# Optimization experiments

Hardware: AMD Instinct MI355X
Metric: run time of the kernel (lower is better)

## Reference

```python
import jax, jax.numpy as jnp
import numpy as np

N, E = 50000, 500000
G_DIM, H1, H2 = 256, 128, 128
N_REL, N_BASES = 8, 30  # 2 * n_speakers**2 with n_speakers=2


def setup_inputs() -> dict:
    key = jax.random.key(0)
    ks = jax.random.split(key, 12)
    inp = {
        "node_features": jax.random.normal(ks[0], (N, G_DIM), jnp.float32),
        "edge_index": jax.random.randint(ks[1], (2, E), 0, N, jnp.int64),
        "edge_norm": jax.random.uniform(ks[2], (E,), jnp.float32),
        "edge_type": jax.random.randint(ks[3], (E,), 0, N_REL, jnp.int64),
        # RGCNConv (basis decomposition) params
        "basis": jax.random.normal(ks[4], (N_BASES, G_DIM, H1), jnp.float32) / np.sqrt(G_DIM),
        "comp": jax.random.normal(ks[5], (N_REL, N_BASES), jnp.float32) / np.sqrt(N_BASES),
        "root": jax.random.normal(ks[6], (G_DIM, H1), jnp.float32) / np.sqrt(G_DIM),
        "bias1": jnp.zeros((H1,), jnp.float32),
        # GATv2Conv params (heads=1)
        "w_l": jax.random.normal(ks[7], (H1, H2), jnp.float32) / np.sqrt(H1),
        "w_r": jax.random.normal(ks[8], (H1, H2), jnp.float32) / np.sqrt(H1),
        "att": jax.random.normal(ks[9], (H2,), jnp.float32) / np.sqrt(H2),
        "bias2": jnp.zeros((H2,), jnp.float32),
    }
    return inp


def reference(node_features, edge_index, edge_norm, edge_type,
              basis, comp, root, bias1, w_l, w_r, att, bias2):
    # NOTE: edge_norm is accepted but unused, matching the original forward.
    src, dst = edge_index[0], edge_index[1]
    n = node_features.shape[0]
    R = comp.shape[0]

    # ---- RGCNConv with basis decomposition, per-relation mean aggregation ----
    Wr = jnp.einsum('rb,bio->rio', comp, basis)            # [R, g_dim, h1]
    xr = jnp.einsum('ni,rio->nro', node_features, Wr)      # [N, R, h1]
    msg = xr[src, edge_type]                               # [E, h1] gather per edge
    seg = dst * R + edge_type                              # segment = (node, relation)
    sums = jax.ops.segment_sum(msg, seg, num_segments=n * R)
    cnts = jax.ops.segment_sum(jnp.ones((msg.shape[0],), msg.dtype), seg, num_segments=n * R)
    mean = sums / jnp.maximum(cnts, 1.0)[:, None]          # per-(node,relation) mean
    agg = mean.reshape(n, R, -1).sum(axis=1)               # sum over relations
    x1 = agg + node_features @ root + bias1                # [N, h1]

    # ---- GATv2Conv (heads=1, add_self_loops=True) ----
    loop = jnp.arange(n, dtype=src.dtype)
    s2 = jnp.concatenate([src, loop])
    d2 = jnp.concatenate([dst, loop])
    xl = x1 @ w_l                                          # source transform [N, h2]
    xrt = x1 @ w_r                                         # target transform [N, h2]
    e = jax.nn.leaky_relu(xl[s2] + xrt[d2], 0.2) @ att     # [E+N] edge scores
    emax = jax.ops.segment_max(e, d2, num_segments=n)      # self-loops => every seg nonempty
    ex = jnp.exp(e - emax[d2])
    denom = jax.ops.segment_sum(ex, d2, num_segments=n)
    alpha = ex / denom[d2]                                 # segment softmax over incoming edges
    out = jax.ops.segment_sum(alpha[:, None] * xl[s2], d2, num_segments=n) + bias2
    return out
```

## Files before the change

### kernel.cpp

```cpp
#include <hip/hip_runtime.h>
#include <hip/hip_bf16.h>
#include <cstdint>
#include <cstddef>

#define NN 50000
#define NE 500000
#define GD 256
#define H1 128
#define H2 128
#define NREL 8
#define NBASES 30
#define XRLD (NREL * H1)
#define NCHUNKS ((NN + 1023) / 1024)

typedef __attribute__((ext_vector_type(8))) short bf16x8;
typedef __attribute__((ext_vector_type(4))) float f32x4;
typedef __attribute__((ext_vector_type(8))) unsigned short u16x8;

__device__ __forceinline__ float lrelu(float x) { return x > 0.f ? x : 0.2f * x; }

__device__ __forceinline__ unsigned short f2bf(float x) {
  union { float f; uint32_t u; } v; v.f = x;
  uint32_t r = v.u + 0x7FFF + ((v.u >> 16) & 1);
  return (unsigned short)(r >> 16);
}
__device__ __forceinline__ float bf2f(unsigned short u) {
  union { uint32_t u; float f; } v; v.u = ((uint32_t)u) << 16;
  return v.f;
}

template <int N>
__device__ __forceinline__ void wait_vmcnt() {
  asm volatile("s_waitcnt vmcnt(%0)" :: "n"(N) : "memory");
}

__device__ __forceinline__ void gload_lds(const unsigned short* gp, unsigned short* lp) {
  __builtin_amdgcn_global_load_lds(
      (const __attribute__((address_space(1))) void*)gp,
      (__attribute__((address_space(3))) void*)lp, 16, 0, 0);
}

__global__ void k_cast(const float* __restrict__ in, unsigned short* __restrict__ out) {
  int i = blockIdx.x * 256 + threadIdx.x;
  const float4* p = (const float4*)(in + (size_t)i * 8);
  float4 a = p[0], b = p[1];
  u16x8 r;
  r[0] = f2bf(a.x); r[1] = f2bf(a.y); r[2] = f2bf(a.z); r[3] = f2bf(a.w);
  r[4] = f2bf(b.x); r[5] = f2bf(b.y); r[6] = f2bf(b.z); r[7] = f2bf(b.w);
  *(u16x8*)(out + (size_t)i * 8) = r;
}

__global__ void k_wr(const float* __restrict__ basis, const float* __restrict__ comp,
                     unsigned short* __restrict__ wrb_t) {
  int idx = blockIdx.x * 256 + threadIdx.x;
  int n = idx >> 8;
  int k = idx & 255;
  int r = n >> 7, o = n & 127;
  float acc = 0.f;
  #pragma unroll
  for (int b = 0; b < NBASES; b++)
    acc += comp[r * NBASES + b] * basis[((size_t)b * GD + k) * H1 + o];
  wrb_t[idx] = f2bf(acc);
}

__global__ void k_prep(const float* __restrict__ root, const float* __restrict__ w_l,
                       const float* __restrict__ w_r, const float* __restrict__ bias1,
                       unsigned short* __restrict__ btf, float* __restrict__ biasv) {
  int idx = blockIdx.x * 256 + threadIdx.x;
  if (idx < 32768) {
    int c = idx >> 7, k = idx & 127;
    float v = (c < H2) ? w_l[k * H2 + c] : w_r[k * H2 + (c - H2)];
    btf[c * 384 + k] = f2bf(v);
  } else if (idx < 98304) {
    int j2 = idx - 32768;
    int c = j2 >> 8, g = j2 & 255;
    float acc = 0.f;
    for (int j = 0; j < H1; j++) {
      float w = (c < H2) ? w_l[j * H2 + c] : w_r[j * H2 + (c - H2)];
      acc += root[g * H1 + j] * w;
    }
    btf[c * 384 + 128 + g] = f2bf(acc);
  } else if (idx < 98560) {
    int c = idx - 98304;
    float acc = 0.f;
    for (int j = 0; j < H1; j++) {
      float w = (c < H2) ? w_l[j * H2 + c] : w_r[j * H2 + (c - H2)];
      acc += bias1[j] * w;
    }
    biasv[c] = acc;
  }
}

template <int K, int WM>
__global__ __launch_bounds__(256, 3)
void k_mgemm(const unsigned short* __restrict__ A, const unsigned short* __restrict__ Bt,
             unsigned short* __restrict__ C, int M, int N, int gx) {
  constexpr int BM = WM * 32;
  constexpr int ACH = BM * 4;
  constexpr int TCH = ACH + 512;
  constexpr int LPT = TCH / 256;
  constexpr int NS = K / 32;
  constexpr int ABUF = BM * 32;
  constexpr int BBUF = 128 * 32;
  extern __shared__ unsigned short lds[];
  const int tid = threadIdx.x;
  const int lane = tid & 63;
  const int wave = tid >> 6;

  const int nwg = gridDim.x;
  const int q = nwg >> 3, r = nwg & 7;
  const int xcd = blockIdx.x & 7, bi = blockIdx.x >> 3;
  const int wg = (xcd < r ? xcd * (q + 1) : r * (q + 1) + (xcd - r) * q) + bi;
  const int bx = wg % gx;
  const int by = wg / gx;
  const int row0 = by * BM;
  const int colb = bx * 128;
  const int wcol = (wave & 1) * 64;
  const int wrow = (wave >> 1) * (WM * 16);
  const int lr = lane & 15;
  const int lko = lane >> 4;

  f32x4 acc[WM][4];
  #pragma unroll
  for (int i = 0; i < WM; i++)
    #pragma unroll
    for (int j = 0; j < 4; j++) acc[i][j] = (f32x4){0.f, 0.f, 0.f, 0.f};

  auto stage = [&](int k0, int b) {
    unsigned short* as = lds + b * ABUF;
    unsigned short* bs = lds + 3 * ABUF + b * BBUF;
    #pragma unroll
    for (int it = 0; it < LPT; it++) {
      int ci = it * 256 + tid;
      if (ci < ACH) {
        int row = ci >> 2, cs = ci & 3;
        int s = (row & 3) ^ ((row >> 2) & 3);
        int gm = row0 + row; if (gm >= M) gm = M - 1;
        gload_lds(A + (size_t)gm * K + k0 + ((cs ^ s) << 3), as + (size_t)ci * 8);
      } else {
        int cj = ci - ACH;
        int row = cj >> 2, cs = cj & 3;
        int s = (row & 3) ^ ((row >> 2) & 3);
        gload_lds(Bt + (size_t)(colb + row) * K + k0 + ((cs ^ s) << 3), bs + (size_t)cj * 8);
      }
    }
  };

  auto compute = [&](int b) {
    const unsigned short* as = lds + b * ABUF;
    const unsigned short* bs = lds + 3 * ABUF + b * BBUF;
    bf16x8 af[WM], bfr[4];
    #pragma unroll
    for (int mb = 0; mb < WM; mb++) {
      int rowL = wrow + mb * 16 + lr;
      int s = (rowL & 3) ^ ((rowL >> 2) & 3);
      af[mb] = *(const bf16x8*)&as[rowL * 32 + ((lko ^ s) << 3)];
    }
    #pragma unroll
    for (int nb = 0; nb < 4; nb++) {
      int colL = wcol + nb * 16 + lr;
      int s = (colL & 3) ^ ((colL >> 2) & 3);
      bfr[nb] = *(const bf16x8*)&bs[colL * 32 + ((lko ^ s) << 3)];
    }
    #pragma unroll
    for (int mb = 0; mb < WM; mb++)
      #pragma unroll
      for (int nb = 0; nb < 4; nb++)
        acc[mb][nb] = __builtin_amdgcn_mfma_f32_16x16x32_bf16(af[mb], bfr[nb], acc[mb][nb], 0, 0, 0);
  };

  stage(0, 0);
  stage(32, 1);
  wait_vmcnt<LPT>();
  __builtin_amdgcn_sched_barrier(0);
  __builtin_amdgcn_s_barrier();
  #pragma unroll
  for (int s = 0; s < NS; s++) {
    if (s + 2 < NS) stage((s + 2) * 32, (s + 2) % 3);
    compute(s % 3);
    if (s + 1 < NS) {
      if (s + 2 < NS) wait_vmcnt<LPT>();
      else            wait_vmcnt<0>();
      __builtin_amdgcn_sched_barrier(0);
      __builtin_amdgcn_s_barrier();
    }
  }

  __syncthreads();
  unsigned short* Cs = lds;
  const int orow = lko * 4;
  #pragma unroll
  for (int mb = 0; mb < WM; mb++) {
    #pragma unroll
    for (int i = 0; i < 4; i++) {
      int row = wrow + mb * 16 + orow + i;
      int sw = (row & 7) << 3;
      #pragma unroll
      for (int nb = 0; nb < 4; nb++) {
        int col = wcol + nb * 16 + lr;
        Cs[row * 128 + (col ^ sw)] = f2bf(acc[mb][nb][i]);
      }
    }
  }
  __syncthreads();
  #pragma unroll
  for (int it = 0; it < BM / 16; it++) {
    int off = it * 256 + tid;
    int row = off >> 4, jb = off & 15;
    int grow = row0 + row;
    if (grow < M) {
      int idx = row * 128 + ((jb * 8) ^ ((row & 7) << 3));
      *(u16x8*)&C[(size_t)grow * N + colb + jb * 8] = *(const u16x8*)&Cs[idx];
    }
  }
}

__global__ __launch_bounds__(256, 3)
void k_fused(const unsigned short* __restrict__ A1, const unsigned short* __restrict__ A2,
             const unsigned short* __restrict__ Bt, const float* __restrict__ biasv,
             unsigned short* __restrict__ C, int M) {
  constexpr int K = 384, NS = 12, LPT = 4;
  extern __shared__ unsigned short lds[];
  const int tid = threadIdx.x;
  const int lane = tid & 63;
  const int wave = tid >> 6;

  const int nwg = gridDim.x;
  const int q = nwg >> 3, r = nwg & 7;
  const int xcd = blockIdx.x & 7, bi = blockIdx.x >> 3;
  const int wg = (xcd < r ? xcd * (q + 1) : r * (q + 1) + (xcd - r) * q) + bi;
  const int bx = wg & 1;
  const int by = wg >> 1;
  const int row0 = by * 128;
  const int colb = bx * 128;
  const int wcol = (wave & 1) * 64;
  const int wrow = (wave >> 1) * 64;
  const int lr = lane & 15;
  const int lko = lane >> 4;

  f32x4 acc[4][4];
  #pragma unroll
  for (int i = 0; i < 4; i++)
    #pragma unroll
    for (int j = 0; j < 4; j++) acc[i][j] = (f32x4){0.f, 0.f, 0.f, 0.f};

  auto stage = [&](int k0, int b) {
    unsigned short* as = lds + b * 4096;
    unsigned short* bs = lds + 3 * 4096 + b * 4096;
    #pragma unroll
    for (int it = 0; it < LPT; it++) {
      int ci = it * 256 + tid;
      if (ci < 512) {
        int row = ci >> 2, cs = ci & 3;
        int s = (row & 3) ^ ((row >> 2) & 3);
        int gm = row0 + row; if (gm >= M) gm = M - 1;
        const unsigned short* gp;
        if (k0 < 128) gp = A1 + (size_t)gm * 128 + k0 + ((cs ^ s) << 3);
        else          gp = A2 + (size_t)gm * 256 + (k0 - 128) + ((cs ^ s) << 3);
        gload_lds(gp, as + (size_t)ci * 8);
      } else {
        int cj = ci - 512;
        int row = cj >> 2, cs = cj & 3;
        int s = (row & 3) ^ ((row >> 2) & 3);
        gload_lds(Bt + (size_t)(colb + row) * K + k0 + ((cs ^ s) << 3), bs + (size_t)cj * 8);
      }
    }
  };

  auto compute = [&](int b) {
    const unsigned short* as = lds + b * 4096;
    const unsigned short* bs = lds + 3 * 4096 + b * 4096;
    bf16x8 af[4], bfr[4];
    #pragma unroll
    for (int mb = 0; mb < 4; mb++) {
      int rowL = wrow + mb * 16 + lr;
      int s = (rowL & 3) ^ ((rowL >> 2) & 3);
      af[mb] = *(const bf16x8*)&as[rowL * 32 + ((lko ^ s) << 3)];
    }
    #pragma unroll
    for (int nb = 0; nb < 4; nb++) {
      int colL = wcol + nb * 16 + lr;
      int s = (colL & 3) ^ ((colL >> 2) & 3);
      bfr[nb] = *(const bf16x8*)&bs[colL * 32 + ((lko ^ s) << 3)];
    }
    #pragma unroll
    for (int mb = 0; mb < 4; mb++)
      #pragma unroll
      for (int nb = 0; nb < 4; nb++)
        acc[mb][nb] = __builtin_amdgcn_mfma_f32_16x16x32_bf16(af[mb], bfr[nb], acc[mb][nb], 0, 0, 0);
  };

  stage(0, 0);
  stage(32, 1);
  wait_vmcnt<LPT>();
  __builtin_amdgcn_sched_barrier(0);
  __builtin_amdgcn_s_barrier();
  #pragma unroll
  for (int s = 0; s < NS; s++) {
    if (s + 2 < NS) stage((s + 2) * 32, (s + 2) % 3);
    compute(s % 3);
    if (s + 1 < NS) {
      if (s + 2 < NS) wait_vmcnt<LPT>();
      else            wait_vmcnt<0>();
      __builtin_amdgcn_sched_barrier(0);
      __builtin_amdgcn_s_barrier();
    }
  }

  __syncthreads();
  unsigned short* Cs = lds;
  const int orow = lko * 4;
  #pragma unroll
  for (int mb = 0; mb < 4; mb++) {
    #pragma unroll
    for (int i = 0; i < 4; i++) {
      int row = wrow + mb * 16 + orow + i;
      int sw = (row & 7) << 3;
      #pragma unroll
      for (int nb = 0; nb < 4; nb++) {
        int col = wcol + nb * 16 + lr;
        Cs[row * 128 + (col ^ sw)] = f2bf(acc[mb][nb][i] + biasv[colb + col]);
      }
    }
  }
  __syncthreads();
  #pragma unroll
  for (int it = 0; it < 8; it++) {
    int off = it * 256 + tid;
    int row = off >> 4, jb = off & 15;
    int grow = row0 + row;
    if (grow < M) {
      int idx = row * 128 + ((jb * 8) ^ ((row & 7) << 3));
      *(u16x8*)&C[(size_t)grow * 256 + colb + jb * 8] = *(const u16x8*)&Cs[idx];
    }
  }
}

__global__ void k_deg(const int* __restrict__ ei, const int* __restrict__ et,
                      int* __restrict__ cnt2) {
  int e = blockIdx.x * 256 + threadIdx.x;
  if (e < NE) atomicAdd(&cnt2[ei[NE + e] * NREL + et[e]], 1);
}

__device__ __forceinline__ int node_deg(const int* cnt2, int n) {
  const int4* p = (const int4*)(cnt2 + n * NREL);
  int4 a = p[0], b = p[1];
  return a.x + a.y + a.z + a.w + b.x + b.y + b.z + b.w;
}

__global__ void k_scan_a(const int* __restrict__ cnt2, int* __restrict__ parts) {
  __shared__ int lds[256];
  int t = threadIdx.x;
  int base = blockIdx.x * 1024 + t * 4;
  int s = 0;
  #pragma unroll
  for (int j = 0; j < 4; j++) s += (base + j < NN) ? node_deg(cnt2, base + j) : 0;
  lds[t] = s;
  __syncthreads();
  for (int st = 128; st > 0; st >>= 1) {
    if (t < st) lds[t] += lds[t + st];
    __syncthreads();
  }
  if (t == 0) parts[blockIdx.x] = lds[0];
}

__global__ void k_scan_b(int* __restrict__ parts) {
  int t = threadIdx.x;
  int v = (t < NCHUNKS) ? parts[t] : 0;
  int x = v;
  #pragma unroll
  for (int off = 1; off < 64; off <<= 1) {
    int y = __shfl_up(x, off, 64);
    if (t >= off) x += y;
  }
  if (t < NCHUNKS) parts[t] = x - v;
}

__global__ void k_scan_c(const int* __restrict__ cnt2, const int* __restrict__ parts,
                         int* __restrict__ rowptr) {
  __shared__ int lds[256];
  int t = threadIdx.x;
  int base = blockIdx.x * 1024 + t * 4;
  int v[4];
  int s = 0;
  #pragma unroll
  for (int j = 0; j < 4; j++) { v[j] = (base + j < NN) ? node_deg(cnt2, base + j) : 0; s += v[j]; }
  lds[t] = s;
  __syncthreads();
  for (int st = 1; st < 256; st <<= 1) {
    int add = (t >= st) ? lds[t - st] : 0;
    __syncthreads();
    lds[t] += add;
    __syncthreads();
  }
  int excl = lds[t] - s;
  int off = parts[blockIdx.x];
  int run = 0;
  #pragma unroll
  for (int j = 0; j < 4; j++) {
    run += v[j];
    if (base + j < NN) rowptr[base + j + 1] = off + excl + run;
  }
  if (blockIdx.x == 0 && t == 0) rowptr[0] = 0;
}

__global__ void k_scatter(const int* __restrict__ ei, const int* __restrict__ et,
                          const int* __restrict__ rowptr, const int* __restrict__ cnt2,
                          int* __restrict__ cursor, int* __restrict__ csr,
                          float* __restrict__ wgt) {
  int e = blockIdx.x * 256 + threadIdx.x;
  if (e < NE) {
    int d = ei[NE + e];
    int r = et[e];
    int pos = atomicAdd(&cursor[d], 1);
    int slot = rowptr[d] + pos;
    csr[slot] = ei[e] | (r << 20);
    wgt[slot] = 1.0f / (float)cnt2[d * NREL + r];
  }
}

__global__ __launch_bounds__(256)
void k_rgcn(const unsigned short* __restrict__ xr, const int* __restrict__ csr2,
            const float* __restrict__ wgt, const int* __restrict__ rowptr,
            unsigned short* __restrict__ agg) {
  int wpair = (blockIdx.x * 256 + threadIdx.x) >> 6;
  int lane = threadIdx.x & 63;
  int hb = lane & 32;
  int l = lane & 31;
  int wid = wpair * 2 + (hb >> 5);
  if (wid >= NN) return;
  int c0 = l * 4;
  float a0 = 0.f, a1 = 0.f, a2 = 0.f, a3 = 0.f;
  int beg = rowptr[wid], end = rowptr[wid + 1];
  for (int j0 = beg; j0 < end; j0 += 32) {
    int nv = end - j0; if (nv > 32) nv = 32;
    int pk = (l < nv) ? csr2[j0 + l] : 0;
    float wk = (l < nv) ? wgt[j0 + l] : 0.f;
    int t = 0;
    for (; t + 8 <= nv; t += 8) {
      uint2 wv[8]; float wz[8];
      #pragma unroll
      for (int z = 0; z < 8; z++) {
        int p = __shfl(pk, hb + t + z, 64);
        wz[z] = __shfl(wk, hb + t + z, 64);
        size_t off = (size_t)(p & 0xFFFFF) * XRLD + (p >> 20) * H1 + c0;
        wv[z] = *(const uint2*)(xr + off);
      }
      #pragma unroll
      for (int z = 0; z < 8; z++) {
        a0 += wz[z] * bf2f((unsigned short)(wv[z].x & 0xffff));
        a1 += wz[z] * bf2f((unsigned short)(wv[z].x >> 16));
        a2 += wz[z] * bf2f((unsigned short)(wv[z].y & 0xffff));
        a3 += wz[z] * bf2f((unsigned short)(wv[z].y >> 16));
      }
    }
    for (; t < nv; t++) {
      int p = __shfl(pk, hb + t, 64);
      float w = __shfl(wk, hb + t, 64);
      size_t off = (size_t)(p & 0xFFFFF) * XRLD + (p >> 20) * H1 + c0;
      uint2 wv = *(const uint2*)(xr + off);
      a0 += w * bf2f((unsigned short)(wv.x & 0xffff));
      a1 += w * bf2f((unsigned short)(wv.x >> 16));
      a2 += w * bf2f((unsigned short)(wv.y & 0xffff));
      a3 += w * bf2f((unsigned short)(wv.y >> 16));
    }
  }
  uint2 packed;
  packed.x = (uint32_t)f2bf(a0) | ((uint32_t)f2bf(a1) << 16);
  packed.y = (uint32_t)f2bf(a2) | ((uint32_t)f2bf(a3) << 16);
  *(uint2*)&agg[(size_t)wid * H1 + c0] = packed;
}

__global__ __launch_bounds__(256)
void k_gat(const unsigned short* __restrict__ xlr, const int* __restrict__ csr2,
           const int* __restrict__ rowptr, const float* __restrict__ att,
           const float* __restrict__ bias2, float* __restrict__ out) {
  int wpair = (blockIdx.x * 256 + threadIdx.x) >> 6;
  int lane = threadIdx.x & 63;
  int hb = lane & 32;
  int l = lane & 31;
  int wid = wpair * 2 + (hb >> 5);
  if (wid >= NN) return;
  int c0 = l * 4;
  float4 at = *(const float4*)(att + c0);
  uint2 wr2 = *(const uint2*)(xlr + (size_t)wid * 256 + 128 + c0);
  float xr0 = bf2f((unsigned short)(wr2.x & 0xffff));
  float xr1 = bf2f((unsigned short)(wr2.x >> 16));
  float xr2 = bf2f((unsigned short)(wr2.y & 0xffff));
  float xr3 = bf2f((unsigned short)(wr2.y >> 16));
  uint2 wv0 = *(const uint2*)(xlr + (size_t)wid * 256 + c0);
  float v0 = bf2f((unsigned short)(wv0.x & 0xffff));
  float v1 = bf2f((unsigned short)(wv0.x >> 16));
  float v2 = bf2f((unsigned short)(wv0.y & 0xffff));
  float v3 = bf2f((unsigned short)(wv0.y >> 16));
  float ep = lrelu(v0 + xr0) * at.x + lrelu(v1 + xr1) * at.y +
             lrelu(v2 + xr2) * at.z + lrelu(v3 + xr3) * at.w;
  #pragma unroll
  for (int off = 16; off > 0; off >>= 1) ep += __shfl_xor(ep, off, 64);
  float m = ep, s = 1.f, o0 = v0, o1 = v1, o2 = v2, o3 = v3;
  int beg = rowptr[wid], end = rowptr[wid + 1];
  for (int j0 = beg; j0 < end; j0 += 32) {
    int nv = end - j0; if (nv > 32) nv = 32;
    int pk = (l < nv) ? csr2[j0 + l] : 0;
    int t = 0;
    for (; t + 8 <= nv; t += 8) {
      float u0[8], u1[8], u2[8], u3[8], p[8];
      #pragma unroll
      for (int z = 0; z < 8; z++) {
        int src = __shfl(pk, hb + t + z, 64) & 0xFFFFF;
        uint2 wu = *(const uint2*)(xlr + (size_t)src * 256 + c0);
        u0[z] = bf2f((unsigned short)(wu.x & 0xffff));
        u1[z] = bf2f((unsigned short)(wu.x >> 16));
        u2[z] = bf2f((unsigned short)(wu.y & 0xffff));
        u3[z] = bf2f((unsigned short)(wu.y >> 16));
      }
      #pragma unroll
      for (int z = 0; z < 8; z++)
        p[z] = lrelu(u0[z] + xr0) * at.x + lrelu(u1[z] + xr1) * at.y +
               lrelu(u2[z] + xr2) * at.z + lrelu(u3[z] + xr3) * at.w;
      #pragma unroll
      for (int off = 16; off > 0; off >>= 1) {
        #pragma unroll
        for (int z = 0; z < 8; z++) p[z] += __shfl_xor(p[z], off, 64);
      }
      float pm = p[0];
      #pragma unroll
      for (int z = 1; z < 8; z++) pm = fmaxf(pm, p[z]);
      float mn = fmaxf(m, pm);
      float sc = __expf(m - mn);
      float e[8];
      #pragma unroll
      for (int z = 0; z < 8; z++) e[z] = __expf(p[z] - mn);
      float es = 0.f, e0 = 0.f, e1 = 0.f, e2 = 0.f, e3 = 0.f;
      #pragma unroll
      for (int z = 0; z < 8; z++) {
        es += e[z]; e0 += e[z] * u0[z]; e1 += e[z] * u1[z];
        e2 += e[z] * u2[z]; e3 += e[z] * u3[z];
      }
      s = s * sc + es;
      o0 = o0 * sc + e0; o1 = o1 * sc + e1;
      o2 = o2 * sc + e2; o3 = o3 * sc + e3;
      m = mn;
    }
    for (; t < nv; t++) {
      int src = __shfl(pk, hb + t, 64) & 0xFFFFF;
      uint2 wu = *(const uint2*)(xlr + (size_t)src * 256 + c0);
      float u0 = bf2f((unsigned short)(wu.x & 0xffff));
      float u1 = bf2f((unsigned short)(wu.x >> 16));
      float u2 = bf2f((unsigned short)(wu.y & 0xffff));
      float u3 = bf2f((unsigned short)(wu.y >> 16));
      float p = lrelu(u0 + xr0) * at.x + lrelu(u1 + xr1) * at.y +
                lrelu(u2 + xr2) * at.z + lrelu(u3 + xr3) * at.w;
      #pragma unroll
      for (int off = 16; off > 0; off >>= 1) p += __shfl_xor(p, off, 64);
      float mn = fmaxf(m, p);
      float sc = __expf(m - mn), w = __expf(p - mn);
      s = s * sc + w;
      o0 = o0 * sc + w * u0; o1 = o1 * sc + w * u1;
      o2 = o2 * sc + w * u2; o3 = o3 * sc + w * u3;
      m = mn;
    }
  }
  float inv = 1.f / s;
  float4 b2 = *(const float4*)(bias2 + c0);
  float4 res = make_float4(o0 * inv + b2.x, o1 * inv + b2.y,
                           o2 * inv + b2.z, o3 * inv + b2.w);
  *(float4*)&out[(size_t)wid * H1 + c0] = res;
}

extern "C" void kernel_launch(void* const* d_in, const int* in_sizes, int n_in,
                              void* d_out, int out_size, void* d_ws, size_t ws_size,
                              hipStream_t stream) {
  const float* nf    = (const float*)d_in[0];
  const int*   ei    = (const int*)d_in[1];
  const int*   et    = (const int*)d_in[3];
  const float* basis = (const float*)d_in[4];
  const float* comp  = (const float*)d_in[5];
  const float* root  = (const float*)d_in[6];
  const float* bias1 = (const float*)d_in[7];
  const float* w_l   = (const float*)d_in[8];
  const float* w_r   = (const float*)d_in[9];
  const float* att   = (const float*)d_in[10];
  const float* bias2 = (const float*)d_in[11];
  float* out = (float*)d_out;

  char* ws = (char*)d_ws;
  unsigned short* xr_bf  = (unsigned short*)ws;
  unsigned short* nf_bf  = (unsigned short*)(ws + 102400000);
  unsigned short* wrb_t  = (unsigned short*)(ws + 128000000);
  unsigned short* btf    = (unsigned short*)(ws + 128524288);
  float*          biasv  = (float*)(ws + 128720896);
  unsigned short* agg_bf = (unsigned short*)(ws + 128721920);
  int*            cursor = (int*)(ws + 141521920);
  int*            cnt2   = cursor + NN;
  int*            rowptr = cnt2 + NN * NREL;
  int*            csr    = rowptr + NN + 1;
  int*            parts  = csr + NE;
  float*          wgt    = (float*)(parts + 64);
  unsigned short* xlr_bf = (unsigned short*)ws;

  hipMemsetAsync(cursor, 0, (1 + NREL) * NN * sizeof(int), stream);

  k_cast<<<(NN * GD / 8) / 256, 256, 0, stream>>>(nf, nf_bf);
  k_wr<<<(XRLD * GD) / 256, 256, 0, stream>>>(basis, comp, wrb_t);
  k_prep<<<(98560 + 255) / 256, 256, 0, stream>>>(root, w_l, w_r, bias1, btf, biasv);

  const int GY128 = (NN + 127) / 128;
  k_mgemm<256, 4><<<8 * GY128, 256, 49152, stream>>>(
      nf_bf, wrb_t, xr_bf, NN, XRLD, 8);

  k_deg<<<(NE + 255) / 256, 256, 0, stream>>>(ei, et, cnt2);
  k_scan_a<<<NCHUNKS, 256, 0, stream>>>(cnt2, parts);
  k_scan_b<<<1, 64, 0, stream>>>(parts);
  k_scan_c<<<NCHUNKS, 256, 0, stream>>>(cnt2, parts, rowptr);
  k_scatter<<<(NE + 255) / 256, 256, 0, stream>>>(ei, et, rowptr, cnt2, cursor, csr, wgt);

  k_rgcn<<<(NN + 7) / 8, 256, 0, stream>>>(xr_bf, csr, wgt, rowptr, agg_bf);

  k_fused<<<2 * GY128, 256, 49152, stream>>>(agg_bf, nf_bf, btf, biasv, xlr_bf, NN);

  k_gat<<<(NN + 7) / 8, 256, 0, stream>>>(xlr_bf, csr, rowptr, att, bias2, out);
}
```

Baseline: 258.6 us.

## Split xl/xrt into separate arrays and merge tail loops into masked batches

The fused GEMM now writes the source and target transforms to two separate [N,128] bf16 buffers instead of one interleaved [N,256] buffer. Random per-edge gathers of xl in the GAT kernel then touch a denser array, which should improve cache locality. Both gather kernels also drop their scalar tail loop and process leftover edges in the same 8-wide batch, masking the unused slots. This adds some wasted loads and exp work on partial batches in exchange for fewer serial steps and better latency hiding.

```diff
diff --git a/kernel.cpp b/kernel.cpp
--- a/kernel.cpp
+++ b/kernel.cpp
@@ -218,7 +218,7 @@
 __global__ __launch_bounds__(256, 3)
 void k_fused(const unsigned short* __restrict__ A1, const unsigned short* __restrict__ A2,
              const unsigned short* __restrict__ Bt, const float* __restrict__ biasv,
-             unsigned short* __restrict__ C, int M) {
+             unsigned short* __restrict__ xl, unsigned short* __restrict__ xrt, int M) {
   constexpr int K = 384, NS = 12, LPT = 4;
   extern __shared__ unsigned short lds[];
   const int tid = threadIdx.x;
@@ -324,6 +324,7 @@
     }
   }
   __syncthreads();
+  unsigned short* Cout = bx ? xrt : xl;
   #pragma unroll
   for (int it = 0; it < 8; it++) {
     int off = it * 256 + tid;
@@ -331,7 +332,7 @@
     int grow = row0 + row;
     if (grow < M) {
       int idx = row * 128 + ((jb * 8) ^ ((row & 7) << 3));
-      *(u16x8*)&C[(size_t)grow * 256 + colb + jb * 8] = *(const u16x8*)&Cs[idx];
+      *(u16x8*)&Cout[(size_t)grow * 128 + jb * 8] = *(const u16x8*)&Cs[idx];
     }
   }
 }
@@ -436,15 +437,18 @@
     int nv = end - j0; if (nv > 32) nv = 32;
     int pk = (l < nv) ? csr2[j0 + l] : 0;
     float wk = (l < nv) ? wgt[j0 + l] : 0.f;
-    int t = 0;
-    for (; t + 8 <= nv; t += 8) {
+    for (int t = 0; t < nv; t += 8) {
       uint2 wv[8]; float wz[8];
       #pragma unroll
       for (int z = 0; z < 8; z++) {
         int p = __shfl(pk, hb + t + z, 64);
         wz[z] = __shfl(wk, hb + t + z, 64);
-        size_t off = (size_t)(p & 0xFFFFF) * XRLD + (p >> 20) * H1 + c0;
-        wv[z] = *(const uint2*)(xr + off);
+        if (t + z < nv) {
+          size_t off = (size_t)(p & 0xFFFFF) * XRLD + (p >> 20) * H1 + c0;
+          wv[z] = *(const uint2*)(xr + off);
+        } else {
+          wv[z] = make_uint2(0, 0);
+        }
       }
       #pragma unroll
       for (int z = 0; z < 8; z++) {
@@ -454,16 +458,6 @@
         a3 += wz[z] * bf2f((unsigned short)(wv[z].y >> 16));
       }
     }
-    for (; t < nv; t++) {
-      int p = __shfl(pk, hb + t, 64);
-      float w = __shfl(wk, hb + t, 64);
-      size_t off = (size_t)(p & 0xFFFFF) * XRLD + (p >> 20) * H1 + c0;
-      uint2 wv = *(const uint2*)(xr + off);
-      a0 += w * bf2f((unsigned short)(wv.x & 0xffff));
-      a1 += w * bf2f((unsigned short)(wv.x >> 16));
-      a2 += w * bf2f((unsigned short)(wv.y & 0xffff));
-      a3 += w * bf2f((unsigned short)(wv.y >> 16));
-    }
   }
   uint2 packed;
   packed.x = (uint32_t)f2bf(a0) | ((uint32_t)f2bf(a1) << 16);
@@ -472,9 +466,10 @@
 }
 
 __global__ __launch_bounds__(256)
-void k_gat(const unsigned short* __restrict__ xlr, const int* __restrict__ csr2,
-           const int* __restrict__ rowptr, const float* __restrict__ att,
-           const float* __restrict__ bias2, float* __restrict__ out) {
+void k_gat(const unsigned short* __restrict__ xl, const unsigned short* __restrict__ xrt,
+           const int* __restrict__ csr2, const int* __restrict__ rowptr,
+           const float* __restrict__ att, const float* __restrict__ bias2,
+           float* __restrict__ out) {
   int wpair = (blockIdx.x * 256 + threadIdx.x) >> 6;
   int lane = threadIdx.x & 63;
   int hb = lane & 32;
@@ -483,12 +478,12 @@
   if (wid >= NN) return;
   int c0 = l * 4;
   float4 at = *(const float4*)(att + c0);
-  uint2 wr2 = *(const uint2*)(xlr + (size_t)wid * 256 + 128 + c0);
+  uint2 wr2 = *(const uint2*)(xrt + (size_t)wid * 128 + c0);
   float xr0 = bf2f((unsigned short)(wr2.x & 0xffff));
   float xr1 = bf2f((unsigned short)(wr2.x >> 16));
   float xr2 = bf2f((unsigned short)(wr2.y & 0xffff));
   float xr3 = bf2f((unsigned short)(wr2.y >> 16));
-  uint2 wv0 = *(const uint2*)(xlr + (size_t)wid * 256 + c0);
+  uint2 wv0 = *(const uint2*)(xl + (size_t)wid * 128 + c0);
   float v0 = bf2f((unsigned short)(wv0.x & 0xffff));
   float v1 = bf2f((unsigned short)(wv0.x >> 16));
   float v2 = bf2f((unsigned short)(wv0.y & 0xffff));
@@ -502,13 +497,14 @@
   for (int j0 = beg; j0 < end; j0 += 32) {
     int nv = end - j0; if (nv > 32) nv = 32;
     int pk = (l < nv) ? csr2[j0 + l] : 0;
-    int t = 0;
-    for (; t + 8 <= nv; t += 8) {
+    for (int t = 0; t < nv; t += 8) {
       float u0[8], u1[8], u2[8], u3[8], p[8];
       #pragma unroll
       for (int z = 0; z < 8; z++) {
         int src = __shfl(pk, hb + t + z, 64) & 0xFFFFF;
-        uint2 wu = *(const uint2*)(xlr + (size_t)src * 256 + c0);
+        uint2 wu;
+        if (t + z < nv) wu = *(const uint2*)(xl + (size_t)src * 128 + c0);
+        else            wu = make_uint2(0, 0);
         u0[z] = bf2f((unsigned short)(wu.x & 0xffff));
         u1[z] = bf2f((unsigned short)(wu.x >> 16));
         u2[z] = bf2f((unsigned short)(wu.y & 0xffff));
@@ -523,6 +519,8 @@
         #pragma unroll
         for (int z = 0; z < 8; z++) p[z] += __shfl_xor(p[z], off, 64);
       }
+      #pragma unroll
+      for (int z = 0; z < 8; z++) if (t + z >= nv) p[z] = -1e30f;
       float pm = p[0];
       #pragma unroll
       for (int z = 1; z < 8; z++) pm = fmaxf(pm, p[z]);
@@ -540,24 +538,6 @@
       s = s * sc + es;
       o0 = o0 * sc + e0; o1 = o1 * sc + e1;
       o2 = o2 * sc + e2; o3 = o3 * sc + e3;
-      m = mn;
-    }
-    for (; t < nv; t++) {
-      int src = __shfl(pk, hb + t, 64) & 0xFFFFF;
-      uint2 wu = *(const uint2*)(xlr + (size_t)src * 256 + c0);
-      float u0 = bf2f((unsigned short)(wu.x & 0xffff));
-      float u1 = bf2f((unsigned short)(wu.x >> 16));
-      float u2 = bf2f((unsigned short)(wu.y & 0xffff));
-      float u3 = bf2f((unsigned short)(wu.y >> 16));
-      float p = lrelu(u0 + xr0) * at.x + lrelu(u1 + xr1) * at.y +
-                lrelu(u2 + xr2) * at.z + lrelu(u3 + xr3) * at.w;
-      #pragma unroll
-      for (int off = 16; off > 0; off >>= 1) p += __shfl_xor(p, off, 64);
-      float mn = fmaxf(m, p);
-      float sc = __expf(m - mn), w = __expf(p - mn);
-      s = s * sc + w;
-      o0 = o0 * sc + w * u0; o1 = o1 * sc + w * u1;
-      o2 = o2 * sc + w * u2; o3 = o3 * sc + w * u3;
       m = mn;
     }
   }
@@ -597,7 +577,8 @@
   int*            csr    = rowptr + NN + 1;
   int*            parts  = csr + NE;
   float*          wgt    = (float*)(parts + 64);
-  unsigned short* xlr_bf = (unsigned short*)ws;
+  unsigned short* xl_bf  = (unsigned short*)ws;
+  unsigned short* xrt_bf = (unsigned short*)(ws + 12800000);
 
   hipMemsetAsync(cursor, 0, (1 + NREL) * NN * sizeof(int), stream);
 
@@ -617,7 +598,7 @@
 
   k_rgcn<<<(NN + 7) / 8, 256, 0, stream>>>(xr_bf, csr, wgt, rowptr, agg_bf);
 
-  k_fused<<<2 * GY128, 256, 49152, stream>>>(agg_bf, nf_bf, btf, biasv, xlr_bf, NN);
-
-  k_gat<<<(NN + 7) / 8, 256, 0, stream>>>(xlr_bf, csr, rowptr, att, bias2, out);
-}
+  k_fused<<<2 * GY128, 256, 49152, stream>>>(agg_bf, nf_bf, btf, biasv, xl_bf, xrt_bf, NN);
+
+  k_gat<<<(NN + 7) / 8, 256, 0, stream>>>(xl_bf, xrt_bf, csr, rowptr, att, bias2, out);
+}
```

Result: faster. 251.4 us (-2.8%).
